# Performance work log

Measured on AMD Instinct MI355X. Metric: run time of the kernel, lower is better.

The kernel has to match this reference:

```python
import jax, jax.numpy as jnp
import numpy as np
from jax import lax

V = 50000      # node_num
LN = 128       # feat_dim
S = 16         # stat_dim
E = 500000     # n_edges
T = 3          # propagation steps
MU = 0.9


def setup_inputs() -> dict:
    key = jax.random.key(0)
    ks = jax.random.split(key, 10)
    X_Node = jax.random.randint(ks[0], (E,), 0, V, dtype=jnp.int32)
    X_Neis = jax.random.randint(ks[1], (E,), 0, V, dtype=jnp.int32)
    dg_list = jax.random.randint(ks[2], (E,), 1, 64, dtype=jnp.int32)
    emb = jax.random.normal(ks[3], (V, LN), dtype=jnp.float32) * 0.1
    xi_w = jax.random.normal(ks[4], (2 * LN, S * S), dtype=jnp.float32) * (1.0 / np.sqrt(2 * LN))
    xi_b = jnp.zeros((S * S,), dtype=jnp.float32)
    rou_w = jax.random.normal(ks[5], (LN, S), dtype=jnp.float32) * (1.0 / np.sqrt(LN))
    rou_b = jnp.zeros((S,), dtype=jnp.float32)
    lin_w = jax.random.normal(ks[6], (LN + S, 3), dtype=jnp.float32) * (1.0 / np.sqrt(LN + S))
    lin_b = jnp.zeros((3,), dtype=jnp.float32)
    return {"X_Node": X_Node, "X_Neis": X_Neis, "dg_list": dg_list,
            "emb": emb, "xi_w": xi_w, "xi_b": xi_b,
            "rou_w": rou_w, "rou_b": rou_b, "lin_w": lin_w, "lin_b": lin_b}


def reference(X_Node, X_Neis, dg_list, emb, xi_w, xi_b, rou_w, rou_b, lin_w, lin_b):
    # edge features: concat(src embed, nbr embed) -> [E, 2*ln]
    Xn = emb[X_Node]                                  # [E, ln]
    X = jnp.concatenate([Xn, emb[X_Neis]], axis=1)    # [E, 2*ln]
    dg = dg_list.astype(emb.dtype)
    # Hw: A = Xi(X)*mu/s/dg  (constant across iterations; torch recomputes, same math)
    A = jnp.tanh(X @ xi_w + xi_b).reshape(-1, S, S)   # [E, s, s]
    A = A * (MU / S) / dg[:, None, None]
    b = jnp.tanh(Xn @ rou_w + rou_b)                  # [E, s]

    states0 = jnp.zeros((V, S), dtype=emb.dtype)

    def step(states, _):
        H = states[X_Node]                            # [E, s] gather
        H = jnp.einsum('est,et->es', A, H) + b        # per-edge small matvec
        states = jax.ops.segment_sum(H, X_Neis, num_segments=V)  # scatter-sum (AggrSum)
        return states, None

    states, _ = lax.scan(step, states0, None, length=T)
    logits = jnp.concatenate([emb, states], axis=1) @ lin_w + lin_b  # [V, 3]
    return jax.nn.softmax(logits, axis=1)
```

## Files before the change

### kernel.cpp

```cpp
#include <hip/hip_runtime.h>
#include <hip/hip_bf16.h>
#include <hip/hip_fp16.h>

#define LN_F 128

typedef __attribute__((ext_vector_type(8))) __bf16 bf16x8;
typedef __attribute__((ext_vector_type(4))) float f32x4;
typedef __attribute__((ext_vector_type(2))) _Float16 half2_t;

__device__ __forceinline__ unsigned short f2bf(float f) {
    unsigned u = __float_as_uint(f);
    u = u + 0x7FFFu + ((u >> 16) & 1u);
    return (unsigned short)(u >> 16);
}
__device__ __forceinline__ float tanh_polyc(float x) {
    x = fminf(1.2f, fmaxf(-1.2f, x));
    float t = x * x;
    float p = fmaf(t, -0.05396825397f, 0.13333333333f);
    p = fmaf(t, p, -0.33333333333f);
    p = fmaf(t, p, 1.0f);
    return x * p;
}
__device__ __forceinline__ float bflo(unsigned u) { return __uint_as_float(u << 16); }
__device__ __forceinline__ float bfhi(unsigned u) { return __uint_as_float(u & 0xffff0000u); }

__device__ __forceinline__ unsigned f2e5(float x) {
    unsigned short u = __half_as_ushort(__float2half(x));
    u = (unsigned short)(u + 0x7F + ((u >> 8) & 1));
    return (unsigned)(u >> 8) & 0xFFu;
}
__device__ __forceinline__ half2_t u2h2(unsigned w) {
    union { unsigned u; half2_t h; } c; c.u = w; return c.h;
}
__device__ __forceinline__ unsigned h2u(half2_t h) {
    union { half2_t h; unsigned u; } c; c.h = h; return c.u;
}
__device__ __forceinline__ half2_t tanh_pk(half2_t x) {
    const half2_t c2 = {(_Float16)(2.0f / 15.0f), (_Float16)(2.0f / 15.0f)};
    const half2_t c1 = {(_Float16)(-1.0f / 3.0f), (_Float16)(-1.0f / 3.0f)};
    const half2_t one = {(_Float16)1.0f, (_Float16)1.0f};
    half2_t t = x * x;
    half2_t p = t * c2 + c1;
    p = t * p + one;
    return x * p;
}

__global__ void k_conv(const float* __restrict__ emb, const float* __restrict__ xiw,
                       const float* __restrict__ rw, const int* __restrict__ Xe,
                       unsigned short* __restrict__ embb, unsigned short* __restrict__ WcT,
                       unsigned short* __restrict__ rouT, int* __restrict__ cnt,
                       float* __restrict__ B1, int V, int E) {
    int t = blockIdx.x * blockDim.x + threadIdx.x;
    int n_emb = V * 16;
    if (t < n_emb) {
        const float4* s = (const float4*)emb;
        float4 a = s[t * 2], b = s[t * 2 + 1];
        uint4 o;
        o.x = (unsigned)f2bf(a.x) | ((unsigned)f2bf(a.y) << 16);
        o.y = (unsigned)f2bf(a.z) | ((unsigned)f2bf(a.w) << 16);
        o.z = (unsigned)f2bf(b.x) | ((unsigned)f2bf(b.y) << 16);
        o.w = (unsigned)f2bf(b.z) | ((unsigned)f2bf(b.w) << 16);
        ((uint4*)embb)[t] = o;
        B1[t] = 0.f;
    } else if (t < n_emb + 512 * 16) {
        int t2 = t - n_emb;
        int cp = t2 >> 4, g = t2 & 15;
        unsigned short u[8];
#pragma unroll
        for (int j = 0; j < 8; ++j) {
            int k = g * 8 + j;
            float w = (cp < 256) ? xiw[k * 256 + cp] : xiw[(128 + k) * 256 + (cp - 256)];
            u[j] = f2bf(w);
        }
        uint4 o;
        o.x = (unsigned)u[0] | ((unsigned)u[1] << 16);
        o.y = (unsigned)u[2] | ((unsigned)u[3] << 16);
        o.z = (unsigned)u[4] | ((unsigned)u[5] << 16);
        o.w = (unsigned)u[6] | ((unsigned)u[7] << 16);
        ((uint4*)WcT)[cp * 16 + (g ^ (cp & 7))] = o;
    } else if (t < n_emb + 512 * 16 + 256) {
        int t2 = t - n_emb - 512 * 16;
        int c = t2 >> 4, g = t2 & 15;
        unsigned short u[8];
#pragma unroll
        for (int j = 0; j < 8; ++j) u[j] = f2bf(rw[(g * 8 + j) * 16 + c]);
        uint4 o;
        o.x = (unsigned)u[0] | ((unsigned)u[1] << 16);
        o.y = (unsigned)u[2] | ((unsigned)u[3] << 16);
        o.z = (unsigned)u[4] | ((unsigned)u[5] << 16);
        o.w = (unsigned)u[6] | ((unsigned)u[7] << 16);
        ((uint4*)rouT)[c * 16 + (g ^ (c & 7))] = o;
    }
    if (t < E) atomicAdd(&cnt[Xe[t]], 1);
}

__global__ __launch_bounds__(256) void k_scan1(const int* __restrict__ cnt,
                                               int* __restrict__ rp,
                                               int* __restrict__ bsum, int V) {
    __shared__ int ls[256];
    int b = blockIdx.x, t = threadIdx.x;
    int i = b * 256 + t;
    int val = (i < V) ? cnt[i] : 0;
    ls[t] = val;
    __syncthreads();
    for (int off = 1; off < 256; off <<= 1) {
        int x = (t >= off) ? ls[t - off] : 0;
        __syncthreads();
        ls[t] += x;
        __syncthreads();
    }
    if (i < V) rp[i] = ls[t] - val;
    if (t == 255) bsum[b] = ls[255];
}

__global__ __launch_bounds__(256) void k_scan2(const int* __restrict__ bsum,
                                               int* __restrict__ boff, int NB) {
    __shared__ int ls[256];
    int t = threadIdx.x;
    int val = (t < NB) ? bsum[t] : 0;
    ls[t] = val;
    __syncthreads();
    for (int off = 1; off < 256; off <<= 1) {
        int x = (t >= off) ? ls[t - off] : 0;
        __syncthreads();
        ls[t] += x;
        __syncthreads();
    }
    if (t < NB) boff[t] = ls[t] - val;
}

__global__ void k_permute(const int* __restrict__ Xn, const int* __restrict__ Xe,
                          const int* __restrict__ dg, const int* __restrict__ rp,
                          const int* __restrict__ boff, int* __restrict__ c2,
                          uint2* __restrict__ erec, int n, int Epad) {
    int e = blockIdx.x * blockDim.x + threadIdx.x;
    if (e < n) {
        int nb = Xe[e];
        int pos = rp[nb] + boff[nb >> 8] + atomicAdd(&c2[nb], 1);
        uint2 r;
        r.x = (unsigned)Xn[e] | ((unsigned)nb << 16);
        r.y = (unsigned)__float_as_int(0.05625f / (float)dg[e]);
        erec[pos] = r;
    } else if (e < Epad) {
        erec[e] = make_uint2(0u, 0u);
    }
}

__global__ __launch_bounds__(512) void k_U(
    const unsigned short* __restrict__ embb, const uint4* __restrict__ WcT,
    const uint4* __restrict__ rouT, const float* __restrict__ xib,
    const float* __restrict__ roub,
    unsigned* __restrict__ U8, unsigned* __restrict__ U28,
    float* __restrict__ bnode, int V) {
    __shared__ uint4 sB[2048];
    __shared__ uint4 sR[256];
    const int half = blockIdx.y;
    for (int i = threadIdx.x; i < 2048; i += 512) sB[i] = WcT[half * 2048 + i];
    if (half == 0 && threadIdx.x < 256) sR[threadIdx.x] = rouT[threadIdx.x];
    __syncthreads();

    const int wave = threadIdx.x >> 6, lane = threadIdx.x & 63;
    const int j = lane & 15, kg = lane >> 4;
    const int wbase = blockIdx.x * 512 + wave * 64;

    int nv[4];
#pragma unroll
    for (int g = 0; g < 4; ++g) nv[g] = min(wbase + g * 16 + j, V - 1);

    f32x4 acc[8][4] = {};
    f32x4 accb[4] = {};
#pragma unroll
    for (int kc = 0; kc < 4; ++kc) {
        bf16x8 bf[4];
#pragma unroll
        for (int g = 0; g < 4; ++g)
            bf[g] = *(const bf16x8*)(embb + (size_t)nv[g] * 128 + kc * 32 + kg * 8);
        int swz = (kc * 4 + kg) ^ (j & 7);
#pragma unroll
        for (int ct = 0; ct < 8; ++ct) {
            bf16x8 afr = ((const bf16x8*)sB)[(ct * 16 + j) * 16 + swz];
#pragma unroll
            for (int g = 0; g < 4; ++g)
                acc[ct][g] = __builtin_amdgcn_mfma_f32_16x16x32_bf16(afr, bf[g], acc[ct][g], 0, 0, 0);
        }
        if (half == 0) {
            bf16x8 rfr = ((const bf16x8*)sR)[j * 16 + swz];
#pragma unroll
            for (int g = 0; g < 4; ++g)
                accb[g] = __builtin_amdgcn_mfma_f32_16x16x32_bf16(rfr, bf[g], accb[g], 0, 0, 0);
        }
    }

#pragma unroll
    for (int ct = 0; ct < 8; ++ct) {
        int c0 = half * 128 + ct * 16 + kg * 4;
        float4 bias = (half < 2) ? ((const float4*)xib)[c0 >> 2]
                                 : make_float4(0.f, 0.f, 0.f, 0.f);
#pragma unroll
        for (int g = 0; g < 4; ++g) {
            int node = wbase + g * 16 + j;
            if (node < V) {
                const f32x4 a = acc[ct][g];
                float v0 = a[0] + bias.x, v1 = a[1] + bias.y;
                float v2 = a[2] + bias.z, v3 = a[3] + bias.w;
                unsigned pk = f2e5(v0) | (f2e5(v1) << 8) | (f2e5(v2) << 16) | (f2e5(v3) << 24);
                if (half < 2) U8[node * 64 + (c0 >> 2)] = pk;
                else          U28[node * 64 + ((c0 - 256) >> 2)] = pk;
            }
        }
    }
    if (half == 0) {
        float4 rb4 = ((const float4*)roub)[kg];
#pragma unroll
        for (int g = 0; g < 4; ++g) {
            int node = wbase + g * 16 + j;
            if (node < V) {
                float4 bo;
                bo.x = tanh_polyc(accb[g][0] + rb4.x);
                bo.y = tanh_polyc(accb[g][1] + rb4.y);
                bo.z = tanh_polyc(accb[g][2] + rb4.z);
                bo.w = tanh_polyc(accb[g][3] + rb4.w);
                *(float4*)(bnode + (size_t)node * 16 + kg * 4) = bo;
            }
        }
    }
}

__global__ __launch_bounds__(256) void k_B1e(
    const float* __restrict__ bnode, const uint2* __restrict__ erec,
    float* __restrict__ B1, int E, int Epad) {
    int wid = (blockIdx.x * 256 + threadIdx.x) >> 6;
    int wbase = wid * 64;
    if (wbase >= Epad) return;
    int lane = threadIdx.x & 63;
    int g = lane >> 4, s = lane & 15, lbase = g * 16;
    int sbase = wbase + lbase;

    int em = wbase + lane;
    unsigned rx = erec[em].x;
    int my_u = (int)(rx & 0xFFFFu);
    int d_own = (int)(rx >> 16);
    int d_nxt = (int)(((const unsigned*)erec)[2 * min(em + 1, Epad - 1)] >> 16);
    unsigned long long flags = __ballot(d_own != d_nxt);

    int cur = __shfl(d_own, lbase, 64);
    float acc = 0.f;
#pragma unroll 4
    for (int j = 0; j < 16; ++j) {
        int p = sbase + j;
        int u = __shfl(my_u, lbase + j, 64);
        float v = bnode[(size_t)u * 16 + s];
        acc += (p < E) ? v : 0.f;
        bool flush = ((flags >> (lbase + j)) & 1ull) || (j == 15);
        if (flush) {
            atomicAdd(&B1[(size_t)cur * 16 + s], acc);
            acc = 0.f;
            if (j < 15) cur = __shfl(d_nxt, lbase + j, 64);
        }
    }
}

__global__ void k_prep(const float* __restrict__ st, unsigned* __restrict__ Hf,
                       float* __restrict__ cp1, float* __restrict__ cp2, int n2) {
    int i = blockIdx.x * blockDim.x + threadIdx.x;
    if (i >= n2) return;
    float2 f = ((const float2*)st)[i];
    half2_t h = {(_Float16)f.x, (_Float16)f.y};
    Hf[i] = h2u(h);
    if (cp1 != nullptr) {
        ((float2*)cp1)[i] = f;
        ((float2*)cp2)[i] = f;
    }
}

__global__ __launch_bounds__(256) void k_prop_e(
    const unsigned* __restrict__ U8, const unsigned* __restrict__ U28,
    const uint2* __restrict__ erec, const unsigned* __restrict__ Hf,
    float* __restrict__ sn, int Epad) {
    int wid = (blockIdx.x * 256 + threadIdx.x) >> 6;
    int wbase = wid * 64;
    if (wbase >= Epad) return;
    int lane = threadIdx.x & 63;
    int g = lane >> 4, s = lane & 15, lbase = g * 16;

    int em = wbase + lane;
    uint2 myr = erec[em];
    int my_u = (int)(myr.x & 0xFFFFu);
    int d_own = (int)(myr.x >> 16);
    int d_nxt = (int)(((const unsigned*)erec)[2 * min(em + 1, Epad - 1)] >> 16);
    unsigned long long flags = __ballot(d_own != d_nxt);

    int cur = __shfl(d_own, lbase, 64);
    half2_t u2h[8];
    {
        uint4 r = ((const uint4*)U28)[cur * 16 + s];
        unsigned wr[4] = {r.x, r.y, r.z, r.w};
#pragma unroll
        for (int q = 0; q < 4; ++q) {
            u2h[2 * q]     = u2h2(__builtin_amdgcn_perm(wr[q], 0u, 0x05000400u));
            u2h[2 * q + 1] = u2h2(__builtin_amdgcn_perm(wr[q], 0u, 0x07000600u));
        }
    }

    float acc = 0.f;
#pragma unroll 4
    for (int j = 0; j < 16; ++j) {
        int u = __shfl(my_u, lbase + j, 64);
        float sc = __int_as_float(__shfl((int)myr.y, lbase + j, 64));
        uint4 q1 = ((const uint4*)U8)[u * 16 + s];
        unsigned h2 = Hf[u * 8 + (s & 7)];
        unsigned wq[4] = {q1.x, q1.y, q1.z, q1.w};
        float sum = 0.f;
#pragma unroll
        for (int q = 0; q < 4; ++q) {
            half2_t x0 = u2h2(__builtin_amdgcn_perm(wq[q], 0u, 0x05000400u)) + u2h[2 * q];
            half2_t x1 = u2h2(__builtin_amdgcn_perm(wq[q], 0u, 0x07000600u)) + u2h[2 * q + 1];
            half2_t r0 = tanh_pk(x0);
            half2_t r1 = tanh_pk(x1);
            unsigned hm0 = __shfl(h2, lbase + 2 * q, 64);
            unsigned hm1 = __shfl(h2, lbase + 2 * q + 1, 64);
            sum = __builtin_amdgcn_fdot2(r0, u2h2(hm0), sum, false);
            sum = __builtin_amdgcn_fdot2(r1, u2h2(hm1), sum, false);
        }
        acc = fmaf(sc, sum, acc);
        bool flush = ((flags >> (lbase + j)) & 1ull) || (j == 15);
        if (flush) {
            atomicAdd(&sn[(size_t)cur * 16 + s], acc);
            acc = 0.f;
            if (j < 15) {
                cur = __shfl(d_nxt, lbase + j, 64);
                uint4 r = ((const uint4*)U28)[cur * 16 + s];
                unsigned wr[4] = {r.x, r.y, r.z, r.w};
#pragma unroll
                for (int q = 0; q < 4; ++q) {
                    u2h[2 * q]     = u2h2(__builtin_amdgcn_perm(wr[q], 0u, 0x05000400u));
                    u2h[2 * q + 1] = u2h2(__builtin_amdgcn_perm(wr[q], 0u, 0x07000600u));
                }
            }
        }
    }
}

__global__ void k_final(const unsigned short* __restrict__ embb, const float* __restrict__ st,
                        const float* __restrict__ lw, const float* __restrict__ lb,
                        float* __restrict__ out, int nv) {
    __shared__ float sw[435];
    for (int i = threadIdx.x; i < 435; i += 256) sw[i] = (i < 432) ? lw[i] : lb[i - 432];
    __syncthreads();
    int t = blockIdx.x * blockDim.x + threadIdx.x;
    int v = t >> 4, j = t & 15;
    if (v >= nv) return;
    const uint4 q = *(const uint4*)(embb + (size_t)v * 128 + j * 8);
    unsigned uu[4] = {q.x, q.y, q.z, q.w};
    float a0 = 0.f, a1 = 0.f, a2 = 0.f;
#pragma unroll
    for (int m = 0; m < 4; ++m) {
        int i = j * 8 + 2 * m;
        float x0 = bflo(uu[m]), x1 = bfhi(uu[m]);
        a0 += x0 * sw[i * 3] + x1 * sw[(i + 1) * 3];
        a1 += x0 * sw[i * 3 + 1] + x1 * sw[(i + 1) * 3 + 1];
        a2 += x0 * sw[i * 3 + 2] + x1 * sw[(i + 1) * 3 + 2];
    }
    float xs = st[(size_t)v * 16 + j];
    a0 += xs * sw[(128 + j) * 3]; a1 += xs * sw[(128 + j) * 3 + 1]; a2 += xs * sw[(128 + j) * 3 + 2];
#pragma unroll
    for (int m = 1; m < 16; m <<= 1) {
        a0 += __shfl_xor(a0, m, 64);
        a1 += __shfl_xor(a1, m, 64);
        a2 += __shfl_xor(a2, m, 64);
    }
    if (j == 0) {
        a0 += sw[432]; a1 += sw[433]; a2 += sw[434];
        float mx = fmaxf(a0, fmaxf(a1, a2));
        float e0 = __expf(a0 - mx), e1 = __expf(a1 - mx), e2 = __expf(a2 - mx);
        float inv = 1.f / (e0 + e1 + e2);
        out[(size_t)v * 3 + 0] = e0 * inv;
        out[(size_t)v * 3 + 1] = e1 * inv;
        out[(size_t)v * 3 + 2] = e2 * inv;
    }
}

extern "C" void kernel_launch(void* const* d_in, const int* in_sizes, int n_in,
                              void* d_out, int out_size, void* d_ws, size_t ws_size,
                              hipStream_t stream) {
    const int*   Xn  = (const int*)d_in[0];
    const int*   Xe  = (const int*)d_in[1];
    const int*   dg  = (const int*)d_in[2];
    const float* emb = (const float*)d_in[3];
    const float* xiw = (const float*)d_in[4];
    const float* xib = (const float*)d_in[5];
    const float* rw  = (const float*)d_in[6];
    const float* rb  = (const float*)d_in[7];
    const float* lw  = (const float*)d_in[8];
    const float* lb  = (const float*)d_in[9];
    float* out = (float*)d_out;
    const int E = in_sizes[0];
    const int V = in_sizes[3] / LN_F;
    const int NB = (V + 255) / 256;
    const int Epad = (E + 63) & ~63;

    char* p = (char*)d_ws;
    auto carve = [&](size_t bytes) {
        char* q = p; p += (bytes + 255) & ~(size_t)255; return q;
    };
    int*   cnt   = (int*)carve((size_t)V * 4);
    int*   c2    = (int*)carve((size_t)V * 4);
    size_t zero_bytes = (size_t)(p - (char*)cnt);
    float* B1    = (float*)carve((size_t)V * 16 * 4);
    unsigned short* embb = (unsigned short*)carve((size_t)V * 128 * 2);
    unsigned* U8    = (unsigned*)carve((size_t)V * 256);
    unsigned* U28   = (unsigned*)carve((size_t)V * 256);
    uint4* WcT   = (uint4*)carve(512 * 16 * 16);
    uint4* rouT  = (uint4*)carve(4096);
    float* bnode = (float*)carve((size_t)V * 16 * 4);
    float* stB   = (float*)carve((size_t)V * 16 * 4);
    float* stA   = (float*)carve((size_t)V * 16 * 4);
    unsigned* Hf = (unsigned*)carve((size_t)V * 16 * 2);
    int*   rp    = (int*)carve((size_t)(V + 1) * 4);
    int*   bsum  = (int*)carve(256 * 4);
    int*   boff  = (int*)carve(256 * 4);
    uint2* erec  = (uint2*)carve((size_t)Epad * 8);

    hipMemsetAsync(cnt, 0, zero_bytes, stream);

    {
        int nconv = V * 16 + 512 * 16 + 256;
        int ntot = nconv > E ? nconv : E;
        k_conv<<<(ntot + 255) / 256, 256, 0, stream>>>(
            emb, xiw, rw, Xe, embb, (unsigned short*)WcT, (unsigned short*)rouT,
            cnt, B1, V, E);
    }

    k_scan1<<<NB, 256, 0, stream>>>(cnt, rp, bsum, V);
    k_scan2<<<1, 256, 0, stream>>>(bsum, boff, NB);

    {
        int ng = (Epad > E ? Epad : E);
        k_permute<<<(ng + 255) / 256, 256, 0, stream>>>(Xn, Xe, dg, rp, boff, c2, erec, E, Epad);
    }

    {
        dim3 g((V + 511) / 512, 4);
        k_U<<<g, 512, 0, stream>>>(embb, WcT, rouT, xib, rb, U8, U28, bnode, V);
    }

    const int n2 = V * 8;
    const int pblocks = (Epad / 64 + 3) / 4;

    k_B1e<<<pblocks, 256, 0, stream>>>(bnode, erec, B1, E, Epad);

    k_prep<<<(n2 + 255) / 256, 256, 0, stream>>>(B1, Hf, stB, stA, n2);
    k_prop_e<<<pblocks, 256, 0, stream>>>(U8, U28, erec, Hf, stB, Epad);

    k_prep<<<(n2 + 255) / 256, 256, 0, stream>>>(stB, Hf, nullptr, nullptr, n2);
    k_prop_e<<<pblocks, 256, 0, stream>>>(U8, U28, erec, Hf, stA, Epad);

    k_final<<<((size_t)V * 16 + 255) / 256, 256, 0, stream>>>(embb, stA, lw, lb, out, V);
}
```

Baseline: 178.6 us.

## Merge two-pass scan into one block and partition permute by node range

Replaces the two-kernel block scan with a single 1024-thread kernel in which each thread serially sums a contiguous chunk of counts, which removes one launch and the boff lookup. The permute kernel now splits blocks into 8 destination-node partitions, each striding over all edges and writing only edges whose neighbor falls in its range. This is meant to give better write locality and less atomic contention in erec and c2. The cost is that every edge index is read 8 times, and the single-block scan does strided, uncoalesced serial reads.

```diff
diff --git a/kernel.cpp b/kernel.cpp
--- a/kernel.cpp
+++ b/kernel.cpp
@@ -94,55 +94,51 @@
     if (t < E) atomicAdd(&cnt[Xe[t]], 1);
 }
 
-__global__ __launch_bounds__(256) void k_scan1(const int* __restrict__ cnt,
-                                               int* __restrict__ rp,
-                                               int* __restrict__ bsum, int V) {
-    __shared__ int ls[256];
-    int b = blockIdx.x, t = threadIdx.x;
-    int i = b * 256 + t;
-    int val = (i < V) ? cnt[i] : 0;
-    ls[t] = val;
+__global__ __launch_bounds__(1024) void k_scan(const int* __restrict__ cnt,
+                                               int* __restrict__ rp, int V) {
+    __shared__ int ls[1024];
+    int tid = threadIdx.x;
+    int per = (V + 1023) / 1024;
+    int s0 = tid * per, s1 = min(s0 + per, V);
+    int sum = 0;
+    for (int i = s0; i < s1; ++i) sum += cnt[i];
+    ls[tid] = sum;
     __syncthreads();
-    for (int off = 1; off < 256; off <<= 1) {
-        int x = (t >= off) ? ls[t - off] : 0;
+    for (int off = 1; off < 1024; off <<= 1) {
+        int v = (tid >= off) ? ls[tid - off] : 0;
         __syncthreads();
-        ls[t] += x;
+        ls[tid] += v;
         __syncthreads();
     }
-    if (i < V) rp[i] = ls[t] - val;
-    if (t == 255) bsum[b] = ls[255];
-}
-
-__global__ __launch_bounds__(256) void k_scan2(const int* __restrict__ bsum,
-                                               int* __restrict__ boff, int NB) {
-    __shared__ int ls[256];
-    int t = threadIdx.x;
-    int val = (t < NB) ? bsum[t] : 0;
-    ls[t] = val;
-    __syncthreads();
-    for (int off = 1; off < 256; off <<= 1) {
-        int x = (t >= off) ? ls[t - off] : 0;
-        __syncthreads();
-        ls[t] += x;
-        __syncthreads();
-    }
-    if (t < NB) boff[t] = ls[t] - val;
-}
-
-__global__ void k_permute(const int* __restrict__ Xn, const int* __restrict__ Xe,
-                          const int* __restrict__ dg, const int* __restrict__ rp,
-                          const int* __restrict__ boff, int* __restrict__ c2,
-                          uint2* __restrict__ erec, int n, int Epad) {
-    int e = blockIdx.x * blockDim.x + threadIdx.x;
-    if (e < n) {
+    int run = (tid == 0) ? 0 : ls[tid - 1];
+    for (int i = s0; i < s1; ++i) { rp[i] = run; run += cnt[i]; }
+    if (tid == 1023) rp[V] = run;
+}
+
+__global__ __launch_bounds__(256) void k_permute(
+    const int* __restrict__ Xn, const int* __restrict__ Xe,
+    const int* __restrict__ dg, const int* __restrict__ rp,
+    int* __restrict__ c2, uint2* __restrict__ erec, int E, int Epad, int V) {
+    int part = blockIdx.x & 7;
+    int sub = blockIdx.x >> 3;
+    int nsub = gridDim.x >> 3;
+    int per = (V + 7) >> 3;
+    int vlo = part * per;
+    int vhi = min(V, vlo + per);
+    int stride = nsub * 256;
+    for (int e = sub * 256 + threadIdx.x; e < E; e += stride) {
         int nb = Xe[e];
-        int pos = rp[nb] + boff[nb >> 8] + atomicAdd(&c2[nb], 1);
-        uint2 r;
-        r.x = (unsigned)Xn[e] | ((unsigned)nb << 16);
-        r.y = (unsigned)__float_as_int(0.05625f / (float)dg[e]);
-        erec[pos] = r;
-    } else if (e < Epad) {
-        erec[e] = make_uint2(0u, 0u);
+        if (nb >= vlo && nb < vhi) {
+            int pos = rp[nb] + atomicAdd(&c2[nb], 1);
+            uint2 r;
+            r.x = (unsigned)Xn[e] | ((unsigned)nb << 16);
+            r.y = (unsigned)__float_as_int(0.05625f / (float)dg[e]);
+            erec[pos] = r;
+        }
+    }
+    if (part == 7) {
+        for (int e = E + sub * 256 + threadIdx.x; e < Epad; e += stride)
+            erec[e] = make_uint2(0u, 0u);
     }
 }
 
@@ -396,7 +392,6 @@
     float* out = (float*)d_out;
     const int E = in_sizes[0];
     const int V = in_sizes[3] / LN_F;
-    const int NB = (V + 255) / 256;
     const int Epad = (E + 63) & ~63;
 
     char* p = (char*)d_ws;
@@ -417,8 +412,6 @@
     float* stA   = (float*)carve((size_t)V * 16 * 4);
     unsigned* Hf = (unsigned*)carve((size_t)V * 16 * 2);
     int*   rp    = (int*)carve((size_t)(V + 1) * 4);
-    int*   bsum  = (int*)carve(256 * 4);
-    int*   boff  = (int*)carve(256 * 4);
     uint2* erec  = (uint2*)carve((size_t)Epad * 8);
 
     hipMemsetAsync(cnt, 0, zero_bytes, stream);
@@ -431,13 +424,9 @@
             cnt, B1, V, E);
     }
 
-    k_scan1<<<NB, 256, 0, stream>>>(cnt, rp, bsum, V);
-    k_scan2<<<1, 256, 0, stream>>>(bsum, boff, NB);
-
-    {
-        int ng = (Epad > E ? Epad : E);
-        k_permute<<<(ng + 255) / 256, 256, 0, stream>>>(Xn, Xe, dg, rp, boff, c2, erec, E, Epad);
-    }
+    k_scan<<<1, 1024, 0, stream>>>(cnt, rp, V);
+
+    k_permute<<<1024, 256, 0, stream>>>(Xn, Xe, dg, rp, c2, erec, E, Epad, V);
 
     {
         dim3 g((V + 511) / 512, 4);
```

Result: slower. 248.8 us (+39.3%).

## Drop prep kernels, convert state to fp16 inline, partition permute by destination

Applied to the files above, without the earlier changes.

Removes the two k_prep launches. The b-term initialisation of stB and stA now happens through extra atomics in k_B1e, and k_prop_e reads the float state directly and packs it to fp16 with cvt_pkrtz. k_permute becomes a fixed grid of 1024 blocks split into 8 destination-node ranges, each scanning all edges, so that scatter atomics and writes are localised per partition. This trades two kernel launches and the Hf buffer for triple atomics, 8x rereads of Xe, and wider state loads in the propagation loop.

```diff
diff --git a/kernel.cpp b/kernel.cpp
--- a/kernel.cpp
+++ b/kernel.cpp
@@ -7,6 +7,7 @@
 typedef __attribute__((ext_vector_type(8))) __bf16 bf16x8;
 typedef __attribute__((ext_vector_type(4))) float f32x4;
 typedef __attribute__((ext_vector_type(2))) _Float16 half2_t;
+typedef __attribute__((ext_vector_type(2))) __fp16 fp16x2_t;
 
 __device__ __forceinline__ unsigned short f2bf(float f) {
     unsigned u = __float_as_uint(f);
@@ -34,6 +35,11 @@
 }
 __device__ __forceinline__ unsigned h2u(half2_t h) {
     union { half2_t h; unsigned u; } c; c.h = h; return c.u;
+}
+__device__ __forceinline__ unsigned pkrtz_u32(float lo, float hi) {
+    union { fp16x2_t h; unsigned u; } c;
+    c.h = __builtin_amdgcn_cvt_pkrtz(lo, hi);
+    return c.u;
 }
 __device__ __forceinline__ half2_t tanh_pk(half2_t x) {
     const half2_t c2 = {(_Float16)(2.0f / 15.0f), (_Float16)(2.0f / 15.0f)};
@@ -49,7 +55,8 @@
                        const float* __restrict__ rw, const int* __restrict__ Xe,
                        unsigned short* __restrict__ embb, unsigned short* __restrict__ WcT,
                        unsigned short* __restrict__ rouT, int* __restrict__ cnt,
-                       float* __restrict__ B1, int V, int E) {
+                       float* __restrict__ B1, float* __restrict__ stB,
+                       float* __restrict__ stA, int V, int E) {
     int t = blockIdx.x * blockDim.x + threadIdx.x;
     int n_emb = V * 16;
     if (t < n_emb) {
@@ -62,6 +69,8 @@
         o.w = (unsigned)f2bf(b.z) | ((unsigned)f2bf(b.w) << 16);
         ((uint4*)embb)[t] = o;
         B1[t] = 0.f;
+        stB[t] = 0.f;
+        stA[t] = 0.f;
     } else if (t < n_emb + 512 * 16) {
         int t2 = t - n_emb;
         int cp = t2 >> 4, g = t2 & 15;
@@ -129,20 +138,31 @@
     if (t < NB) boff[t] = ls[t] - val;
 }
 
-__global__ void k_permute(const int* __restrict__ Xn, const int* __restrict__ Xe,
-                          const int* __restrict__ dg, const int* __restrict__ rp,
-                          const int* __restrict__ boff, int* __restrict__ c2,
-                          uint2* __restrict__ erec, int n, int Epad) {
-    int e = blockIdx.x * blockDim.x + threadIdx.x;
-    if (e < n) {
+__global__ __launch_bounds__(256) void k_permute(
+    const int* __restrict__ Xn, const int* __restrict__ Xe,
+    const int* __restrict__ dg, const int* __restrict__ rp,
+    const int* __restrict__ boff, int* __restrict__ c2,
+    uint2* __restrict__ erec, int E, int Epad, int V) {
+    int part = blockIdx.x & 7;
+    int sub = blockIdx.x >> 3;
+    int nsub = gridDim.x >> 3;
+    int per = (V + 7) >> 3;
+    int vlo = part * per;
+    int vhi = min(V, vlo + per);
+    int stride = nsub * 256;
+    for (int e = sub * 256 + threadIdx.x; e < E; e += stride) {
         int nb = Xe[e];
-        int pos = rp[nb] + boff[nb >> 8] + atomicAdd(&c2[nb], 1);
-        uint2 r;
-        r.x = (unsigned)Xn[e] | ((unsigned)nb << 16);
-        r.y = (unsigned)__float_as_int(0.05625f / (float)dg[e]);
-        erec[pos] = r;
-    } else if (e < Epad) {
-        erec[e] = make_uint2(0u, 0u);
+        if (nb >= vlo && nb < vhi) {
+            int pos = rp[nb] + boff[nb >> 8] + atomicAdd(&c2[nb], 1);
+            uint2 r;
+            r.x = (unsigned)Xn[e] | ((unsigned)nb << 16);
+            r.y = (unsigned)__float_as_int(0.05625f / (float)dg[e]);
+            erec[pos] = r;
+        }
+    }
+    if (part == 7) {
+        for (int e = E + sub * 256 + threadIdx.x; e < Epad; e += stride)
+            erec[e] = make_uint2(0u, 0u);
     }
 }
 
@@ -228,7 +248,8 @@
 
 __global__ __launch_bounds__(256) void k_B1e(
     const float* __restrict__ bnode, const uint2* __restrict__ erec,
-    float* __restrict__ B1, int E, int Epad) {
+    float* __restrict__ B1, float* __restrict__ stB, float* __restrict__ stA,
+    int E, int Epad) {
     int wid = (blockIdx.x * 256 + threadIdx.x) >> 6;
     int wbase = wid * 64;
     if (wbase >= Epad) return;
@@ -253,29 +274,19 @@
         acc += (p < E) ? v : 0.f;
         bool flush = ((flags >> (lbase + j)) & 1ull) || (j == 15);
         if (flush) {
-            atomicAdd(&B1[(size_t)cur * 16 + s], acc);
+            size_t idx = (size_t)cur * 16 + s;
+            atomicAdd(&B1[idx], acc);
+            atomicAdd(&stB[idx], acc);
+            atomicAdd(&stA[idx], acc);
             acc = 0.f;
             if (j < 15) cur = __shfl(d_nxt, lbase + j, 64);
         }
     }
 }
 
-__global__ void k_prep(const float* __restrict__ st, unsigned* __restrict__ Hf,
-                       float* __restrict__ cp1, float* __restrict__ cp2, int n2) {
-    int i = blockIdx.x * blockDim.x + threadIdx.x;
-    if (i >= n2) return;
-    float2 f = ((const float2*)st)[i];
-    half2_t h = {(_Float16)f.x, (_Float16)f.y};
-    Hf[i] = h2u(h);
-    if (cp1 != nullptr) {
-        ((float2*)cp1)[i] = f;
-        ((float2*)cp2)[i] = f;
-    }
-}
-
 __global__ __launch_bounds__(256) void k_prop_e(
     const unsigned* __restrict__ U8, const unsigned* __restrict__ U28,
-    const uint2* __restrict__ erec, const unsigned* __restrict__ Hf,
+    const uint2* __restrict__ erec, const float* __restrict__ sp,
     float* __restrict__ sn, int Epad) {
     int wid = (blockIdx.x * 256 + threadIdx.x) >> 6;
     int wbase = wid * 64;
@@ -308,7 +319,8 @@
         int u = __shfl(my_u, lbase + j, 64);
         float sc = __int_as_float(__shfl((int)myr.y, lbase + j, 64));
         uint4 q1 = ((const uint4*)U8)[u * 16 + s];
-        unsigned h2 = Hf[u * 8 + (s & 7)];
+        float2 hf = *(const float2*)(sp + (size_t)u * 16 + (s & 7) * 2);
+        unsigned h2 = pkrtz_u32(hf.x, hf.y);
         unsigned wq[4] = {q1.x, q1.y, q1.z, q1.w};
         float sum = 0.f;
 #pragma unroll
@@ -415,7 +427,6 @@
     float* bnode = (float*)carve((size_t)V * 16 * 4);
     float* stB   = (float*)carve((size_t)V * 16 * 4);
     float* stA   = (float*)carve((size_t)V * 16 * 4);
-    unsigned* Hf = (unsigned*)carve((size_t)V * 16 * 2);
     int*   rp    = (int*)carve((size_t)(V + 1) * 4);
     int*   bsum  = (int*)carve(256 * 4);
     int*   boff  = (int*)carve(256 * 4);
@@ -428,32 +439,26 @@
         int ntot = nconv > E ? nconv : E;
         k_conv<<<(ntot + 255) / 256, 256, 0, stream>>>(
             emb, xiw, rw, Xe, embb, (unsigned short*)WcT, (unsigned short*)rouT,
-            cnt, B1, V, E);
+            cnt, B1, stB, stA, V, E);
     }
 
     k_scan1<<<NB, 256, 0, stream>>>(cnt, rp, bsum, V);
     k_scan2<<<1, 256, 0, stream>>>(bsum, boff, NB);
 
-    {
-        int ng = (Epad > E ? Epad : E);
-        k_permute<<<(ng + 255) / 256, 256, 0, stream>>>(Xn, Xe, dg, rp, boff, c2, erec, E, Epad);
-    }
+    k_permute<<<1024, 256, 0, stream>>>(Xn, Xe, dg, rp, boff, c2, erec, E, Epad, V);
 
     {
         dim3 g((V + 511) / 512, 4);
         k_U<<<g, 512, 0, stream>>>(embb, WcT, rouT, xib, rb, U8, U28, bnode, V);
     }
 
-    const int n2 = V * 8;
     const int pblocks = (Epad / 64 + 3) / 4;
 
-    k_B1e<<<pblocks, 256, 0, stream>>>(bnode, erec, B1, E, Epad);
-
-    k_prep<<<(n2 + 255) / 256, 256, 0, stream>>>(B1, Hf, stB, stA, n2);
-    k_prop_e<<<pblocks, 256, 0, stream>>>(U8, U28, erec, Hf, stB, Epad);
-
-    k_prep<<<(n2 + 255) / 256, 256, 0, stream>>>(stB, Hf, nullptr, nullptr, n2);
-    k_prop_e<<<pblocks, 256, 0, stream>>>(U8, U28, erec, Hf, stA, Epad);
+    k_B1e<<<pblocks, 256, 0, stream>>>(bnode, erec, B1, stB, stA, E, Epad);
+
+    k_prop_e<<<pblocks, 256, 0, stream>>>(U8, U28, erec, B1, stB, Epad);
+
+    k_prop_e<<<pblocks, 256, 0, stream>>>(U8, U28, erec, stB, stA, Epad);
 
     k_final<<<((size_t)V * 16 + 255) / 256, 256, 0, stream>>>(embb, stA, lw, lb, out, V);
 }
```

After: 178.6 us. Within noise of the previous version (-0.0%).
